# Kernel tuning notes

Hardware: AMD Instinct MI355X
Metric: run time of the kernel (lower is better)

The kernel has to match this reference:

```python
import jax, jax.numpy as jnp
import numpy as np

N_NODES = 100000
N_EDGES = 3200000  # avg degree 32
D_IN = 256
D_OUT = 256


def setup_inputs() -> dict:
    key = jax.random.key(0)
    k1, k2, k3, k4 = jax.random.split(key, 4)
    x = jax.random.normal(k1, (N_NODES, D_IN), dtype=jnp.float32)
    # nn.Linear(in, out, bias=False): weight shape [out, in]
    W = jax.random.normal(k2, (D_OUT, D_IN), dtype=jnp.float32) / np.sqrt(D_IN).astype(np.float32)
    bias = jnp.zeros((D_OUT,), dtype=jnp.float32)
    rows = jax.random.randint(k3, (N_EDGES,), 0, N_NODES, dtype=jnp.int32)
    cols = jax.random.randint(k4, (N_EDGES,), 0, N_NODES, dtype=jnp.int32)
    return {"x": x, "W": W, "bias": bias, "rows": rows, "cols": cols}


def reference(x, W, bias, rows, cols):
    # aggr == 'planetoid-gcn-residual' branch; dropout p=0 (identity).
    n = x.shape[0]
    h = x @ W.T + bias                                      # [N, D_out]
    # adj_t.sum(dim=-1): per-row degree of binary adjacency
    deg = jax.ops.segment_sum(jnp.ones(rows.shape, x.dtype), rows, num_segments=n)
    norm = jax.lax.rsqrt(1.0 + deg)[:, None]                # [N, 1]
    h = norm * h
    # spmm_add(adj_t, h)[i] = sum_{(i,j) in E} h[j]
    agg = jax.ops.segment_sum(h[cols], rows, num_segments=n)
    h = agg + h
    return norm * h
```

## Files before the change

kernel.cpp:

```cpp
#include <hip/hip_runtime.h>
#include <hip/hip_fp16.h>
#include <stdint.h>


#define THREADS 256
#define NB 256
#define B3_EDGES 8192

typedef _Float16 half8 __attribute__((ext_vector_type(8)));
typedef float floatx4 __attribute__((ext_vector_type(4)));

__global__ __launch_bounds__(THREADS) void bucket_count(
    const int* __restrict__ rows, int* __restrict__ bcnt, int E, int nbuck) {
    __shared__ int h[NB];
    h[threadIdx.x] = 0;
    __syncthreads();
    int nquad  = E >> 2;
    int stride = gridDim.x * THREADS;
    for (int q = blockIdx.x * THREADS + threadIdx.x; q < nquad; q += stride) {
        int4 r = ((const int4*)rows)[q];
        atomicAdd(&h[r.x >> 9], 1);
        atomicAdd(&h[r.y >> 9], 1);
        atomicAdd(&h[r.z >> 9], 1);
        atomicAdd(&h[r.w >> 9], 1);
    }
    if (blockIdx.x == 0)
        for (int e = (nquad << 2) + threadIdx.x; e < E; e += THREADS)
            atomicAdd(&h[rows[e] >> 9], 1);
    __syncthreads();
    int v = h[threadIdx.x];
    if (threadIdx.x < nbuck && v) atomicAdd(&bcnt[threadIdx.x], v);
}

__global__ __launch_bounds__(THREADS) void bucket_scan(
    const int* __restrict__ bcnt, int* __restrict__ boff, int* __restrict__ bcur,
    int nbuck, int E) {
    __shared__ int s[THREADS];
    int tid = threadIdx.x;
    int v = (tid < nbuck) ? bcnt[tid] : 0;
    s[tid] = v;
    __syncthreads();
    for (int off = 1; off < THREADS; off <<= 1) {
        int t = (tid >= off) ? s[tid - off] : 0;
        __syncthreads();
        s[tid] += t;
        __syncthreads();
    }
    int excl = s[tid] - v;
    if (tid < nbuck) { boff[tid] = excl; bcur[tid] = excl; }
    if (tid == 0) boff[nbuck] = E;
}

__global__ __launch_bounds__(THREADS) void bucket_scatter(
    const int* __restrict__ rows, const int* __restrict__ cols,
    int* __restrict__ bcur, uint32_t* __restrict__ buf, int E, int nbuck) {
    __shared__ uint32_t staged[B3_EDGES];
    __shared__ int h[NB], lo[NB], gb[NB], hc[NB];
    int tid = threadIdx.x;
    h[tid] = 0; hc[tid] = 0;
    __syncthreads();
    int e0 = blockIdx.x * B3_EDGES;
    int e1 = e0 + B3_EDGES; if (e1 > E) e1 = E;
    for (int e = e0 + tid; e < e1; e += THREADS)
        atomicAdd(&h[rows[e] >> 9], 1);
    __syncthreads();
    int v = h[tid];
    lo[tid] = v;
    __syncthreads();
    for (int off = 1; off < NB; off <<= 1) {
        int t = (tid >= off) ? lo[tid - off] : 0;
        __syncthreads();
        lo[tid] += t;
        __syncthreads();
    }
    int excl = lo[tid] - v;
    __syncthreads();
    lo[tid] = excl;
    gb[tid] = (tid < nbuck && v) ? atomicAdd(&bcur[tid], v) : 0;
    __syncthreads();
    for (int e = e0 + tid; e < e1; e += THREADS) {
        int r = rows[e];
        int c = cols[e];
        int b = r >> 9;
        int p = lo[b] + atomicAdd(&hc[b], 1);
        staged[p] = ((uint32_t)(r & 511) << 17) | (uint32_t)c;
    }
    __syncthreads();
    int wid = tid >> 6, lane = tid & 63;
    for (int b = wid; b < nbuck; b += 4) {
        int cnt = h[b], src = lo[b], dst = gb[b];
        for (int i = lane; i < cnt; i += 64)
            buf[dst + i] = staged[src + i];
    }
}

__global__ __launch_bounds__(THREADS) void csr_finalize(
    const uint32_t* __restrict__ buf, const int* __restrict__ boff,
    int* __restrict__ rs, int* __restrict__ csr, int n, int E) {
    int b   = blockIdx.x;
    int tid = threadIdx.x;
    __shared__ int h[512], base[512], s1[THREADS];
    h[tid] = 0; h[tid + 256] = 0;
    __syncthreads();
    int s = boff[b], e = boff[b + 1];
    for (int i = s + tid; i < e; i += THREADS)
        atomicAdd(&h[buf[i] >> 17], 1);
    __syncthreads();
    int a0 = h[2 * tid], a1 = h[2 * tid + 1];
    s1[tid] = a0 + a1;
    __syncthreads();
    for (int off = 1; off < THREADS; off <<= 1) {
        int t = (tid >= off) ? s1[tid - off] : 0;
        __syncthreads();
        s1[tid] += t;
        __syncthreads();
    }
    int eps = s1[tid] - (a0 + a1);
    base[2 * tid]     = s + eps;
    base[2 * tid + 1] = s + eps + a0;
    __syncthreads();
#pragma unroll
    for (int j = 0; j < 2; j++) {
        int rl  = tid + j * 256;
        int row = (b << 9) + rl;
        if (row < n) rs[row] = base[rl];
        h[rl] = 0;
    }
    if (b == 0 && tid == 0) rs[n] = E;
    __syncthreads();
    for (int i = s + tid; i < e; i += THREADS) {
        uint32_t v = buf[i];
        int rl = v >> 17;
        int c  = v & 0x1FFFF;
        int p  = base[rl] + atomicAdd(&h[rl], 1);
        csr[p] = c;
    }
}

__global__ void make_bswz(const float* __restrict__ W, half8* __restrict__ Bswz) {
    int t = blockIdx.x * THREADS + threadIdx.x;
    int n_tile = t >> 9;
    int k_step = (t >> 6) & 7;
    int lane   = t & 63;
    int q = lane >> 4, m16 = lane & 15;
    const float* src = W + (size_t)(n_tile * 16 + m16) * 256 + k_step * 32 + q * 8;
    half8 h;
#pragma unroll
    for (int j = 0; j < 8; j++) h[j] = (_Float16)src[j];
    Bswz[t] = h;
}

__device__ __forceinline__ int As_swz(int b) {
    return b ^ ((((b >> 10) & 7) ^ (((b >> 8) & 1) << 3)) << 4);
}

__global__ __launch_bounds__(THREADS) void gemm_mfma(
    const float* __restrict__ x, const half8* __restrict__ Bswz,
    const float* __restrict__ bias, const int* __restrict__ rs,
    _Float16* __restrict__ h16, int n) {
    __shared__ _Float16 As[4 * 8 * 64 * 8];
    int tid  = threadIdx.x;
    int row0 = blockIdx.x * 64;

#pragma unroll
    for (int i = 0; i < 16; i++) {
        int flat = i * THREADS + tid;
        int r  = flat >> 6;
        int k  = (flat & 63) * 4;
        float4 v;
        if (row0 + r < n) v = *(const float4*)(x + (size_t)(row0 + r) * 256 + k);
        else { v.x = 0.f; v.y = 0.f; v.z = 0.f; v.w = 0.f; }
        int m_sub  = r >> 4;
        int k_step = k >> 5;
        int q      = (k >> 3) & 3;
        int j      = k & 7;
        int lane_w = (r & 15) + (q << 4);
        int entry  = (m_sub * 8 + k_step) * 64 + lane_w;
        union { _Float16 h[4]; uint2 u; } pk;
        pk.h[0] = (_Float16)v.x; pk.h[1] = (_Float16)v.y;
        pk.h[2] = (_Float16)v.z; pk.h[3] = (_Float16)v.w;
        *(uint2*)((char*)As + As_swz(entry * 16 + (j << 1))) = pk.u;
    }
    __syncthreads();

    int w    = tid >> 6;
    int lane = tid & 63;

    floatx4 acc[4][4];
#pragma unroll
    for (int ms = 0; ms < 4; ms++)
#pragma unroll
        for (int nn = 0; nn < 4; nn++) {
            acc[ms][nn][0] = 0.f; acc[ms][nn][1] = 0.f;
            acc[ms][nn][2] = 0.f; acc[ms][nn][3] = 0.f;
        }

    for (int ks = 0; ks < 8; ks++) {
        half8 bfrag[4];
#pragma unroll
        for (int nn = 0; nn < 4; nn++)
            bfrag[nn] = Bswz[((w * 4 + nn) * 8 + ks) * 64 + lane];
        half8 afrag[4];
#pragma unroll
        for (int ms = 0; ms < 4; ms++)
            afrag[ms] = *(const half8*)((char*)As +
                            As_swz(((ms * 8 + ks) * 64 + lane) * 16));
#pragma unroll
        for (int ms = 0; ms < 4; ms++)
#pragma unroll
            for (int nn = 0; nn < 4; nn++)
                acc[ms][nn] = __builtin_amdgcn_mfma_f32_16x16x32_f16(
                    afrag[ms], bfrag[nn], acc[ms][nn], 0, 0, 0);
    }

    int rgrp = lane >> 4;
    int cl   = lane & 15;
#pragma unroll
    for (int ms = 0; ms < 4; ms++) {
        int rbase = row0 + ms * 16 + rgrp * 4;
        float nrm[4];
#pragma unroll
        for (int i = 0; i < 4; i++) {
            int r = rbase + i;
            nrm[i] = (r < n) ? rsqrtf(1.0f + (float)(rs[r + 1] - rs[r])) : 0.f;
        }
#pragma unroll
        for (int nn = 0; nn < 4; nn++) {
            int col = w * 64 + nn * 16 + cl;
            float bb = bias[col];
#pragma unroll
            for (int i = 0; i < 4; i++) {
                int r = rbase + i;
                if (r < n)
                    h16[(size_t)r * 256 + col] =
                        (_Float16)((acc[ms][nn][i] + bb) * nrm[i]);
            }
        }
    }
}

__global__ __launch_bounds__(THREADS) void agg_half(
    const _Float16* __restrict__ h16, const int* __restrict__ csr_col,
    const int* __restrict__ rs, float* __restrict__ out, int n, int halfsel) {
    int row = blockIdx.x * 4 + (threadIdx.x >> 6);
    if (row >= n) return;
    int lane = threadIdx.x & 63;
    int g    = lane >> 4;
    int l16  = lane & 15;
    int off  = halfsel * 128 + l16 * 8;
    const _Float16* hb = h16 + off;

    int s   = rs[row];
    int end = rs[row + 1];

    float acc[8] = {0.f, 0.f, 0.f, 0.f, 0.f, 0.f, 0.f, 0.f};
    if (g == 0) {
        half8 v = *(const half8*)(hb + (size_t)row * 256);
#pragma unroll
        for (int j = 0; j < 8; j++) acc[j] = (float)v[j];
    }

    int e = s + g;
    for (; e + 4 < end; e += 8) {
        int c0 = csr_col[e];
        int c1 = csr_col[e + 4];
        half8 v0 = *(const half8*)(hb + (size_t)c0 * 256);
        half8 v1 = *(const half8*)(hb + (size_t)c1 * 256);
#pragma unroll
        for (int j = 0; j < 8; j++) acc[j] += (float)v0[j] + (float)v1[j];
    }
    for (; e < end; e += 4) {
        int c = csr_col[e];
        half8 v = *(const half8*)(hb + (size_t)c * 256);
#pragma unroll
        for (int j = 0; j < 8; j++) acc[j] += (float)v[j];
    }

#pragma unroll
    for (int j = 0; j < 8; j++) acc[j] += __shfl_down(acc[j], 32);
#pragma unroll
    for (int j = 0; j < 8; j++) acc[j] += __shfl_down(acc[j], 16);

    if (g == 0) {
        float nrm = rsqrtf(1.0f + (float)(end - s));
        floatx4 o0, o1;
        o0[0] = acc[0] * nrm; o0[1] = acc[1] * nrm; o0[2] = acc[2] * nrm; o0[3] = acc[3] * nrm;
        o1[0] = acc[4] * nrm; o1[1] = acc[5] * nrm; o1[2] = acc[6] * nrm; o1[3] = acc[7] * nrm;
        float* dst = out + (size_t)row * 256 + off;
        __builtin_nontemporal_store(o0, (floatx4*)dst);
        __builtin_nontemporal_store(o1, (floatx4*)(dst + 4));
    }
}

extern "C" void kernel_launch(void* const* d_in, const int* in_sizes, int n_in,
                              void* d_out, int out_size, void* d_ws, size_t ws_size,
                              hipStream_t stream) {
    const float* x    = (const float*)d_in[0];
    const float* W    = (const float*)d_in[1];
    const float* bias = (const float*)d_in[2];
    const int*   rows = (const int*)d_in[3];
    const int*   cols = (const int*)d_in[4];

    const int D = 256;
    int n = in_sizes[0] / D;
    int E = in_sizes[3];
    int nbuck = (n + 511) >> 9;

    char* p = (char*)d_ws;
    auto alignup = [](size_t v) { return (v + 255) & ~(size_t)255; };
    _Float16* h16 = (_Float16*)p; p += alignup((size_t)n * D * sizeof(_Float16));
    int*   rs     = (int*)p;    p += alignup((size_t)(n + 1) * sizeof(int));
    int*   csr    = (int*)p;    p += alignup((size_t)E * sizeof(int));
    half8* Bswz   = (half8*)p;  p += alignup((size_t)8192 * sizeof(half8));
    int*   bcnt   = (int*)p;    p += alignup((size_t)NB * sizeof(int));
    int*   boff   = (int*)p;    p += alignup((size_t)(NB + 1) * sizeof(int));
    int*   bcur   = (int*)p;    p += alignup((size_t)NB * sizeof(int));

    uint32_t* buf = (uint32_t*)h16;

    hipMemsetAsync(bcnt, 0, (size_t)nbuck * sizeof(int), stream);

    bucket_count<<<256, THREADS, 0, stream>>>(rows, bcnt, E, nbuck);
    bucket_scan<<<1, THREADS, 0, stream>>>(bcnt, boff, bcur, nbuck, E);

    int b3blocks = (E + B3_EDGES - 1) / B3_EDGES;
    bucket_scatter<<<b3blocks, THREADS, 0, stream>>>(rows, cols, bcur, buf, E, nbuck);

    csr_finalize<<<nbuck, THREADS, 0, stream>>>(buf, boff, rs, csr, n, E);

    make_bswz<<<32, THREADS, 0, stream>>>(W, Bswz);

    int gblocks = (n + 63) / 64;
    gemm_mfma<<<gblocks, THREADS, 0, stream>>>(x, Bswz, bias, rs, h16, n);

    int ablocks = (n + 3) / 4;
    agg_half<<<ablocks, THREADS, 0, stream>>>(h16, csr, rs, (float*)d_out, n, 0);
    agg_half<<<ablocks, THREADS, 0, stream>>>(h16, csr, rs, (float*)d_out, n, 1);
}
```

Measured before the change: 548.8 us.

## Aggregate full rows in 8 row-chunk launches and use 256-row CSR buckets

```diff
diff --git a/kernel.cpp b/kernel.cpp
--- a/kernel.cpp
+++ b/kernel.cpp
@@ -4,7 +4,7 @@
 
 
 #define THREADS 256
-#define NB 256
+#define NB 512
 #define B3_EDGES 8192
 
 typedef _Float16 half8 __attribute__((ext_vector_type(8)));
@@ -13,41 +13,46 @@
 __global__ __launch_bounds__(THREADS) void bucket_count(
     const int* __restrict__ rows, int* __restrict__ bcnt, int E, int nbuck) {
     __shared__ int h[NB];
-    h[threadIdx.x] = 0;
+    h[threadIdx.x] = 0; h[threadIdx.x + 256] = 0;
     __syncthreads();
     int nquad  = E >> 2;
     int stride = gridDim.x * THREADS;
     for (int q = blockIdx.x * THREADS + threadIdx.x; q < nquad; q += stride) {
         int4 r = ((const int4*)rows)[q];
-        atomicAdd(&h[r.x >> 9], 1);
-        atomicAdd(&h[r.y >> 9], 1);
-        atomicAdd(&h[r.z >> 9], 1);
-        atomicAdd(&h[r.w >> 9], 1);
+        atomicAdd(&h[r.x >> 8], 1);
+        atomicAdd(&h[r.y >> 8], 1);
+        atomicAdd(&h[r.z >> 8], 1);
+        atomicAdd(&h[r.w >> 8], 1);
     }
     if (blockIdx.x == 0)
         for (int e = (nquad << 2) + threadIdx.x; e < E; e += THREADS)
-            atomicAdd(&h[rows[e] >> 9], 1);
-    __syncthreads();
-    int v = h[threadIdx.x];
-    if (threadIdx.x < nbuck && v) atomicAdd(&bcnt[threadIdx.x], v);
+            atomicAdd(&h[rows[e] >> 8], 1);
+    __syncthreads();
+    for (int b = threadIdx.x; b < nbuck; b += THREADS) {
+        int v = h[b];
+        if (v) atomicAdd(&bcnt[b], v);
+    }
 }
 
 __global__ __launch_bounds__(THREADS) void bucket_scan(
     const int* __restrict__ bcnt, int* __restrict__ boff, int* __restrict__ bcur,
     int nbuck, int E) {
-    __shared__ int s[THREADS];
+    __shared__ int s1[THREADS];
     int tid = threadIdx.x;
-    int v = (tid < nbuck) ? bcnt[tid] : 0;
-    s[tid] = v;
+    int b0 = 2 * tid, b1 = 2 * tid + 1;
+    int v0 = (b0 < nbuck) ? bcnt[b0] : 0;
+    int v1 = (b1 < nbuck) ? bcnt[b1] : 0;
+    s1[tid] = v0 + v1;
     __syncthreads();
     for (int off = 1; off < THREADS; off <<= 1) {
-        int t = (tid >= off) ? s[tid - off] : 0;
-        __syncthreads();
-        s[tid] += t;
-        __syncthreads();
-    }
-    int excl = s[tid] - v;
-    if (tid < nbuck) { boff[tid] = excl; bcur[tid] = excl; }
+        int t = (tid >= off) ? s1[tid - off] : 0;
+        __syncthreads();
+        s1[tid] += t;
+        __syncthreads();
+    }
+    int excl = s1[tid] - (v0 + v1);
+    if (b0 < nbuck) { boff[b0] = excl;      bcur[b0] = excl; }
+    if (b1 < nbuck) { boff[b1] = excl + v0; bcur[b1] = excl + v0; }
     if (tid == 0) boff[nbuck] = E;
 }
 
@@ -55,35 +60,39 @@
     const int* __restrict__ rows, const int* __restrict__ cols,
     int* __restrict__ bcur, uint32_t* __restrict__ buf, int E, int nbuck) {
     __shared__ uint32_t staged[B3_EDGES];
-    __shared__ int h[NB], lo[NB], gb[NB], hc[NB];
+    __shared__ int h[NB], lo[NB], gb[NB], hc[NB], s1[THREADS];
     int tid = threadIdx.x;
-    h[tid] = 0; hc[tid] = 0;
+    h[tid] = 0; h[tid + 256] = 0;
     __syncthreads();
     int e0 = blockIdx.x * B3_EDGES;
     int e1 = e0 + B3_EDGES; if (e1 > E) e1 = E;
     for (int e = e0 + tid; e < e1; e += THREADS)
-        atomicAdd(&h[rows[e] >> 9], 1);
-    __syncthreads();
-    int v = h[tid];
-    lo[tid] = v;
-    __syncthreads();
-    for (int off = 1; off < NB; off <<= 1) {
-        int t = (tid >= off) ? lo[tid - off] : 0;
-        __syncthreads();
-        lo[tid] += t;
-        __syncthreads();
-    }
-    int excl = lo[tid] - v;
-    __syncthreads();
-    lo[tid] = excl;
-    gb[tid] = (tid < nbuck && v) ? atomicAdd(&bcur[tid], v) : 0;
+        atomicAdd(&h[rows[e] >> 8], 1);
+    __syncthreads();
+    int a0 = h[2 * tid], a1 = h[2 * tid + 1];
+    s1[tid] = a0 + a1;
+    __syncthreads();
+    for (int off = 1; off < THREADS; off <<= 1) {
+        int t = (tid >= off) ? s1[tid - off] : 0;
+        __syncthreads();
+        s1[tid] += t;
+        __syncthreads();
+    }
+    int eps = s1[tid] - (a0 + a1);
+    lo[2 * tid]     = eps;
+    lo[2 * tid + 1] = eps + a0;
+    for (int b = tid; b < NB; b += THREADS) {
+        int v = h[b];
+        gb[b] = (b < nbuck && v) ? atomicAdd(&bcur[b], v) : 0;
+        hc[b] = 0;
+    }
     __syncthreads();
     for (int e = e0 + tid; e < e1; e += THREADS) {
         int r = rows[e];
         int c = cols[e];
-        int b = r >> 9;
+        int b = r >> 8;
         int p = lo[b] + atomicAdd(&hc[b], 1);
-        staged[p] = ((uint32_t)(r & 511) << 17) | (uint32_t)c;
+        staged[p] = ((uint32_t)(r & 255) << 17) | (uint32_t)c;
     }
     __syncthreads();
     int wid = tid >> 6, lane = tid & 63;
@@ -99,15 +108,15 @@
     int* __restrict__ rs, int* __restrict__ csr, int n, int E) {
     int b   = blockIdx.x;
     int tid = threadIdx.x;
-    __shared__ int h[512], base[512], s1[THREADS];
-    h[tid] = 0; h[tid + 256] = 0;
+    __shared__ int h[256], base[256], s1[THREADS];
+    h[tid] = 0;
     __syncthreads();
     int s = boff[b], e = boff[b + 1];
     for (int i = s + tid; i < e; i += THREADS)
         atomicAdd(&h[buf[i] >> 17], 1);
     __syncthreads();
-    int a0 = h[2 * tid], a1 = h[2 * tid + 1];
-    s1[tid] = a0 + a1;
+    int v = h[tid];
+    s1[tid] = v;
     __syncthreads();
     for (int off = 1; off < THREADS; off <<= 1) {
         int t = (tid >= off) ? s1[tid - off] : 0;
@@ -115,25 +124,19 @@
         s1[tid] += t;
         __syncthreads();
     }
-    int eps = s1[tid] - (a0 + a1);
-    base[2 * tid]     = s + eps;
-    base[2 * tid + 1] = s + eps + a0;
-    __syncthreads();
-#pragma unroll
-    for (int j = 0; j < 2; j++) {
-        int rl  = tid + j * 256;
-        int row = (b << 9) + rl;
-        if (row < n) rs[row] = base[rl];
-        h[rl] = 0;
-    }
+    int myBase = s + s1[tid] - v;
+    base[tid] = myBase;
+    int row = (b << 8) + tid;
+    if (row < n) rs[row] = myBase;
+    h[tid] = 0;
     if (b == 0 && tid == 0) rs[n] = E;
     __syncthreads();
     for (int i = s + tid; i < e; i += THREADS) {
-        uint32_t v = buf[i];
-        int rl = v >> 17;
-        int c  = v & 0x1FFFF;
-        int p  = base[rl] + atomicAdd(&h[rl], 1);
-        csr[p] = c;
+        uint32_t p = buf[i];
+        int rl = p >> 17;
+        int c  = p & 0x1FFFF;
+        int q  = base[rl] + atomicAdd(&h[rl], 1);
+        csr[q] = c;
     }
 }
 
@@ -239,49 +242,46 @@
     }
 }
 
-__global__ __launch_bounds__(THREADS) void agg_half(
+__global__ __launch_bounds__(THREADS) void agg_rows(
     const _Float16* __restrict__ h16, const int* __restrict__ csr_col,
-    const int* __restrict__ rs, float* __restrict__ out, int n, int halfsel) {
-    int row = blockIdx.x * 4 + (threadIdx.x >> 6);
-    if (row >= n) return;
+    const int* __restrict__ rs, float* __restrict__ out, int r0, int r1) {
+    int row = r0 + blockIdx.x * 4 + (threadIdx.x >> 6);
+    if (row >= r1) return;
     int lane = threadIdx.x & 63;
-    int g    = lane >> 4;
-    int l16  = lane & 15;
-    int off  = halfsel * 128 + l16 * 8;
-    const _Float16* hb = h16 + off;
+    int half = lane >> 5;
+    int l32  = lane & 31;
+    int off  = l32 * 8;
 
     int s   = rs[row];
     int end = rs[row + 1];
 
     float acc[8] = {0.f, 0.f, 0.f, 0.f, 0.f, 0.f, 0.f, 0.f};
-    if (g == 0) {
-        half8 v = *(const half8*)(hb + (size_t)row * 256);
+    if (half == 0) {
+        half8 v = *(const half8*)(h16 + (size_t)row * 256 + off);
 #pragma unroll
         for (int j = 0; j < 8; j++) acc[j] = (float)v[j];
     }
 
-    int e = s + g;
-    for (; e + 4 < end; e += 8) {
+    int e = s + half;
+    for (; e + 2 < end; e += 4) {
         int c0 = csr_col[e];
-        int c1 = csr_col[e + 4];
-        half8 v0 = *(const half8*)(hb + (size_t)c0 * 256);
-        half8 v1 = *(const half8*)(hb + (size_t)c1 * 256);
+        int c1 = csr_col[e + 2];
+        half8 v0 = *(const half8*)(h16 + (size_t)c0 * 256 + off);
+        half8 v1 = *(const half8*)(h16 + (size_t)c1 * 256 + off);
 #pragma unroll
         for (int j = 0; j < 8; j++) acc[j] += (float)v0[j] + (float)v1[j];
     }
-    for (; e < end; e += 4) {
+    for (; e < end; e += 2) {
         int c = csr_col[e];
-        half8 v = *(const half8*)(hb + (size_t)c * 256);
+        half8 v = *(const half8*)(h16 + (size_t)c * 256 + off);
 #pragma unroll
         for (int j = 0; j < 8; j++) acc[j] += (float)v[j];
     }
 
 #pragma unroll
     for (int j = 0; j < 8; j++) acc[j] += __shfl_down(acc[j], 32);
-#pragma unroll
-    for (int j = 0; j < 8; j++) acc[j] += __shfl_down(acc[j], 16);
-
-    if (g == 0) {
+
+    if (half == 0) {
         float nrm = rsqrtf(1.0f + (float)(end - s));
         floatx4 o0, o1;
         o0[0] = acc[0] * nrm; o0[1] = acc[1] * nrm; o0[2] = acc[2] * nrm; o0[3] = acc[3] * nrm;
@@ -304,7 +304,7 @@
     const int D = 256;
     int n = in_sizes[0] / D;
     int E = in_sizes[3];
-    int nbuck = (n + 511) >> 9;
+    int nbuck = (n + 255) >> 8;
 
     char* p = (char*)d_ws;
     auto alignup = [](size_t v) { return (v + 255) & ~(size_t)255; };
@@ -333,7 +333,12 @@
     int gblocks = (n + 63) / 64;
     gemm_mfma<<<gblocks, THREADS, 0, stream>>>(x, Bswz, bias, rs, h16, n);
 
-    int ablocks = (n + 3) / 4;
-    agg_half<<<ablocks, THREADS, 0, stream>>>(h16, csr, rs, (float*)d_out, n, 0);
-    agg_half<<<ablocks, THREADS, 0, stream>>>(h16, csr, rs, (float*)d_out, n, 1);
-}
+    int chunk = (n + 7) / 8;
+    for (int d = 0; d < 8; ++d) {
+        int a0 = d * chunk;
+        int a1 = a0 + chunk; if (a1 > n) a1 = n;
+        if (a0 >= a1) break;
+        int ablocks = (a1 - a0 + 3) / 4;
+        agg_rows<<<ablocks, THREADS, 0, stream>>>(h16, csr, rs, (float*)d_out, a0, a1);
+    }
+}
```

Result: slower. 595.8 us (+8.6%).
